# Performance work log

Hardware: AMD Instinct MI355X
Metric: run time of the kernel (lower is better)

## Reference

```python
import jax, jax.numpy as jnp
import numpy as np

POS_RATIO = 0.5
EPS = 1e-6


def setup_inputs() -> dict:
    key = jax.random.key(0)
    k1, k2, k3, k4 = jax.random.split(key, 4)
    N, C, D, H, W = 8, 256, 8, 16, 16
    q = jax.random.normal(k1, (N, C, D, H, W), dtype=jnp.float32)
    k = jax.random.normal(k2, (N, C, D, H, W), dtype=jnp.float32)
    # coords: (x0, y0, z0, x1, y1, z1) with lower-right > upper-left
    uq = jax.random.uniform(k3, (N, 3), dtype=jnp.float32) * 0.5
    uk = jax.random.uniform(k4, (N, 3), dtype=jnp.float32) * 0.5
    coord_q = jnp.concatenate([uq, uq + 0.5], axis=1)
    coord_k = jnp.concatenate([uk, uk + 0.5], axis=1)
    return {"q": q, "k": k, "coord_q": coord_q, "coord_k": coord_k}


def _centers(coord, D, H, W):
    """Per-batch voxel-center coordinates. coord: [N,6]. Returns cx, cy, cz each [N, D*H*W], plus bin diag [N]."""
    bw = (coord[:, 3] - coord[:, 0]) / W  # [N]
    bh = (coord[:, 4] - coord[:, 1]) / H
    bd = (coord[:, 5] - coord[:, 2]) / D
    gz, gy, gx = jnp.meshgrid(jnp.arange(D, dtype=coord.dtype),
                              jnp.arange(H, dtype=coord.dtype),
                              jnp.arange(W, dtype=coord.dtype), indexing="ij")
    gx = (gx + 0.5).reshape(-1)[None, :]  # [1, DHW]
    gy = (gy + 0.5).reshape(-1)[None, :]
    gz = (gz + 0.5).reshape(-1)[None, :]
    cx = gx * bw[:, None] + coord[:, 0][:, None]
    cy = gy * bh[:, None] + coord[:, 1][:, None]
    cz = gz * bd[:, None] + coord[:, 2][:, None]
    diag = jnp.sqrt(bw ** 2 + bh ** 2 + bd ** 2)  # [N]
    return cx, cy, cz, diag


def reference(q, k, coord_q, coord_k):
    N, C, D, H, W = q.shape
    qf = q.reshape(N, C, -1)  # [N, C, P], P = D*H*W
    kf = k.reshape(N, C, -1)
    cqx, cqy, cqz, q_diag = _centers(coord_q, D, H, W)
    ckx, cky, ckz, k_diag = _centers(coord_k, D, H, W)
    max_diag = jnp.maximum(q_diag, k_diag)  # [N]
    # pairwise center distance, normalized by max bin diagonal: [N, P, P]
    dist = jnp.sqrt((cqx[:, :, None] - ckx[:, None, :]) ** 2
                    + (cqy[:, :, None] - cky[:, None, :]) ** 2
                    + (cqz[:, :, None] - ckz[:, None, :]) ** 2) / max_diag[:, None, None]
    pos_mask = jax.lax.stop_gradient((dist < POS_RATIO).astype(q.dtype))
    # logit[n, p, p'] = sum_c q[n,c,p] * k[n,c,p']
    logit = jnp.einsum("ncp,ncq->npq", qf, kf)
    loss = (logit * pos_mask).sum((-2, -1)) / (pos_mask.sum((-2, -1)) + EPS)  # [N]
    return -2.0 * loss.mean()
```

## Files before the change

### kernel.cpp

```cpp
#include <hip/hip_runtime.h>
#include <cstdint>
#include <cstddef>

#define NB 8
#define CH 256
#define DD 8
#define HH 16
#define WW 16
#define PP 2048

#define OFF_DPART 8192

__device__ __forceinline__ int z_window(float czq, float bdk, float k2, float maxd) {
    float lim = 0.500060f * maxd;
    int zk0 = -1;
    #pragma unroll
    for (int zk = 0; zk < DD; ++zk) {
        float czk = __fadd_rn(__fmul_rn(__fadd_rn((float)zk, 0.5f), bdk), k2);
        bool feas = fabsf(__fsub_rn(czq, czk)) < lim;
        if (feas && zk0 < 0) zk0 = zk;
    }
    if (zk0 > DD - 2) zk0 = DD - 2;
    return zk0;
}

#define CC 8
__global__ __launch_bounds__(256) void fused_kernel(
    const float* __restrict__ q, const float* __restrict__ k,
    const float* __restrict__ coord_q, const float* __restrict__ coord_k,
    float* __restrict__ partial, float* __restrict__ dpart)
{
    __shared__ float klds[CC][512];
    __shared__ float redf[256];
    __shared__ int   redi[256];

    int t  = threadIdx.x;
    int cg = blockIdx.x;
    int zq = blockIdx.y;
    int n  = blockIdx.z;
    int flat = (n * 8 + zq) * 32 + cg;
    int c0 = cg * CC;

    const float* cq = coord_q + n * 6;
    const float* ck = coord_k + n * 6;
    float q0 = cq[0], q1 = cq[1], q2 = cq[2];
    float k0 = ck[0], k1 = ck[1], k2 = ck[2];
    float bwq = __fdiv_rn(__fsub_rn(cq[3], q0), (float)WW);
    float bhq = __fdiv_rn(__fsub_rn(cq[4], q1), (float)HH);
    float bdq = __fdiv_rn(__fsub_rn(cq[5], q2), (float)DD);
    float bwk = __fdiv_rn(__fsub_rn(ck[3], k0), (float)WW);
    float bhk = __fdiv_rn(__fsub_rn(ck[4], k1), (float)HH);
    float bdk = __fdiv_rn(__fsub_rn(ck[5], k2), (float)DD);
    float diagq = __fsqrt_rn(__fadd_rn(__fadd_rn(__fmul_rn(bwq, bwq), __fmul_rn(bhq, bhq)),
                                       __fmul_rn(bdq, bdq)));
    float diagk = __fsqrt_rn(__fadd_rn(__fadd_rn(__fmul_rn(bwk, bwk), __fmul_rn(bhk, bhk)),
                                       __fmul_rn(bdk, bdk)));
    float maxd = fmaxf(diagq, diagk);
    float cqz = __fadd_rn(__fmul_rn(__fadd_rn((float)zq, 0.5f), bdq), q2);

    int zk0 = z_window(cqz, bdk, k2, maxd);
    if (zk0 < 0) {
        if (t == 0) {
            partial[flat] = 0.0f;
            if (cg == 0) dpart[n * 8 + zq] = 0.0f;
        }
        return;
    }
    int base_p = zk0 << 8;

    {
        const float* ksrc = k + ((size_t)(n * CH + c0)) * PP + base_p;
        #pragma unroll
        for (int i = 0; i < 4; ++i) {
            int f = i * 256 + t;
            int c = f >> 7;
            int u = (f & 127) << 2;
            float4 v = *(const float4*)(ksrc + (size_t)c * PP + u);
            klds[c][u + 0] = v.x;
            klds[c][u + 1] = v.y;
            klds[c][u + 2] = v.z;
            klds[c][u + 3] = v.w;
        }
    }
    __syncthreads();

    int ix = t & 15, iy = (t >> 4) & 15;
    float cqx = __fadd_rn(__fmul_rn(__fadd_rn((float)ix, 0.5f), bwq), q0);
    float cqy = __fadd_rn(__fmul_rn(__fadd_rn((float)iy, 0.5f), bhq), q1);

    float lim = 0.500060f * maxd;
    float tx = (cqx - k0) / bwk - 0.5f;
    float ty = (cqy - k1) / bhk - 0.5f;
    float rx = lim / bwk + 0.03f;
    float ry = lim / bhk + 0.03f;
    int jx0 = (int)ceilf(tx - rx);  if (jx0 < 0) jx0 = 0;
    int jx1 = (int)floorf(tx + rx); if (jx1 > WW - 1) jx1 = WW - 1;
    int jy0 = (int)ceilf(ty - ry);  if (jy0 < 0) jy0 = 0;
    int jy1 = (int)floorf(ty + ry); if (jy1 > HH - 1) jy1 = HH - 1;

    float half_maxd = 0.5f * maxd;
    float thr2 = half_maxd * half_maxd * 1.001f;

    float s[CC];
    #pragma unroll
    for (int c = 0; c < CC; ++c) s[c] = 0.0f;
    int cnt = 0;

    for (int dzI = 0; dzI < 2; ++dzI) {
        int jz = zk0 + dzI;
        float ckz = __fadd_rn(__fmul_rn(__fadd_rn((float)jz, 0.5f), bdk), k2);
        float dz  = __fsub_rn(cqz, ckz);
        float dz2 = __fmul_rn(dz, dz);
        for (int jy = jy0; jy <= jy1; ++jy) {
            float cky = __fadd_rn(__fmul_rn(__fadd_rn((float)jy, 0.5f), bhk), k1);
            float dy  = __fsub_rn(cqy, cky);
            float dy2 = __fmul_rn(dy, dy);
            for (int jx = jx0; jx <= jx1; ++jx) {
                float ckx = __fadd_rn(__fmul_rn(__fadd_rn((float)jx, 0.5f), bwk), k0);
                float dx  = __fsub_rn(cqx, ckx);
                float dx2 = __fmul_rn(dx, dx);
                float d2  = __fadd_rn(__fadd_rn(dx2, dy2), dz2);
                bool pos = false;
                if (d2 < thr2) {
                    float dist = __fdiv_rn(__fsqrt_rn(d2), maxd);
                    pos = dist < 0.5f;
                }
                if (pos) {
                    ++cnt;
                    int idx = (dzI << 8) + (jy << 4) + jx;
                    #pragma unroll
                    for (int c = 0; c < CC; ++c)
                        s[c] += klds[c][idx];
                }
            }
        }
    }

    int p = (zq << 8) + t;
    float acc = 0.0f;
    const float* qcol = q + ((size_t)(n * CH + c0)) * PP + p;
    #pragma unroll
    for (int c = 0; c < CC; ++c)
        acc += qcol[(size_t)c * PP] * s[c];

    redf[t] = acc;
    redi[t] = cnt;
    __syncthreads();
    for (int off = 128; off > 0; off >>= 1) {
        if (t < off) { redf[t] += redf[t + off]; redi[t] += redi[t + off]; }
        __syncthreads();
    }
    if (t == 0) {
        partial[flat] = redf[0];
        if (cg == 0) dpart[n * 8 + zq] = (float)redi[0];
    }
}

__global__ __launch_bounds__(512) void final_kernel(const float* __restrict__ partial,
                                                    const float* __restrict__ dpart,
                                                    float* __restrict__ out)
{
    __shared__ float numsh[NB];
    __shared__ float densh[NB];
    int t = threadIdx.x;
    int n = t >> 6, lane = t & 63;

    float sp = 0.0f;
    #pragma unroll
    for (int i = 0; i < 4; ++i)
        sp += partial[n * 256 + i * 64 + lane];
    float sc = (lane < 8) ? dpart[n * 8 + lane] : 0.0f;
    for (int off = 32; off > 0; off >>= 1) {
        sp += __shfl_down(sp, off, 64);
        sc += __shfl_down(sc, off, 64);
    }
    if (lane == 0) { numsh[n] = sp; densh[n] = sc; }
    __syncthreads();
    if (t == 0) {
        float r = 0.0f;
        for (int i = 0; i < NB; ++i)
            r += numsh[i] / (densh[i] + 1e-6f);
        out[0] = -2.0f * (r / (float)NB);
    }
}

extern "C" void kernel_launch(void* const* d_in, const int* in_sizes, int n_in,
                              void* d_out, int out_size, void* d_ws, size_t ws_size,
                              hipStream_t stream) {
    const float* q       = (const float*)d_in[0];
    const float* k       = (const float*)d_in[1];
    const float* coord_q = (const float*)d_in[2];
    const float* coord_k = (const float*)d_in[3];
    float* out = (float*)d_out;

    char* w = (char*)d_ws;
    float* partial = (float*)w;
    float* dpart   = (float*)(w + OFF_DPART);

    fused_kernel<<<dim3(CH / CC, DD, NB), 256, 0, stream>>>(q, k, coord_q, coord_k,
                                                            partial, dpart);
    final_kernel<<<1, 512, 0, stream>>>(partial, dpart, out);
}
```

Before: 82.57 us.

## Double channels per block, prefetch q early, replace LDS reduction with wave shuffles

Doubles the channels handled per block from 8 to 16, which halves the grid and doubles per-block work. It also reuses each thread's neighbour-window distance computation across more channels. The q values are loaded into registers before the k tile is staged, so their global-load latency overlaps the LDS fill and the window search. The shared-memory tree reduction with its many barriers is replaced by per-wave shuffle reductions that write four partials per block, and the final kernel is adjusted to match. The cost is more registers and LDS per block, which can lower occupancy, and fewer blocks (1024) to spread across CUs.

```diff
diff --git a/kernel.cpp b/kernel.cpp
--- a/kernel.cpp
+++ b/kernel.cpp
@@ -9,7 +9,7 @@
 #define WW 16
 #define PP 2048
 
-#define OFF_DPART 8192
+#define OFF_DPART 16384
 
 __device__ __forceinline__ int z_window(float czq, float bdk, float k2, float maxd) {
     float lim = 0.500060f * maxd;
@@ -24,21 +24,21 @@
     return zk0;
 }
 
-#define CC 8
+#define CC 16
 __global__ __launch_bounds__(256) void fused_kernel(
     const float* __restrict__ q, const float* __restrict__ k,
     const float* __restrict__ coord_q, const float* __restrict__ coord_k,
     float* __restrict__ partial, float* __restrict__ dpart)
 {
     __shared__ float klds[CC][512];
-    __shared__ float redf[256];
-    __shared__ int   redi[256];
 
     int t  = threadIdx.x;
+    int wv = t >> 6;
+    int lane = t & 63;
     int cg = blockIdx.x;
     int zq = blockIdx.y;
     int n  = blockIdx.z;
-    int flat = (n * 8 + zq) * 32 + cg;
+    int flat = (n * 8 + zq) * 16 + cg;
     int c0 = cg * CC;
 
     const float* cq = coord_q + n * 6;
@@ -60,18 +60,27 @@
 
     int zk0 = z_window(cqz, bdk, k2, maxd);
     if (zk0 < 0) {
-        if (t == 0) {
-            partial[flat] = 0.0f;
-            if (cg == 0) dpart[n * 8 + zq] = 0.0f;
+        if (lane == 0) {
+            partial[flat * 4 + wv] = 0.0f;
+            if (cg == 0) dpart[(n * 8 + zq) * 4 + wv] = 0.0f;
         }
         return;
     }
     int base_p = zk0 << 8;
+
+    int p = (zq << 8) + t;
+    float qv[CC];
+    {
+        const float* qcol = q + ((size_t)(n * CH + c0)) * PP + p;
+        #pragma unroll
+        for (int c = 0; c < CC; ++c)
+            qv[c] = qcol[(size_t)c * PP];
+    }
 
     {
         const float* ksrc = k + ((size_t)(n * CH + c0)) * PP + base_p;
         #pragma unroll
-        for (int i = 0; i < 4; ++i) {
+        for (int i = 0; i < 8; ++i) {
             int f = i * 256 + t;
             int c = f >> 7;
             int u = (f & 127) << 2;
@@ -136,23 +145,20 @@
         }
     }
 
-    int p = (zq << 8) + t;
     float acc = 0.0f;
-    const float* qcol = q + ((size_t)(n * CH + c0)) * PP + p;
     #pragma unroll
     for (int c = 0; c < CC; ++c)
-        acc += qcol[(size_t)c * PP] * s[c];
-
-    redf[t] = acc;
-    redi[t] = cnt;
-    __syncthreads();
-    for (int off = 128; off > 0; off >>= 1) {
-        if (t < off) { redf[t] += redf[t + off]; redi[t] += redi[t + off]; }
-        __syncthreads();
-    }
-    if (t == 0) {
-        partial[flat] = redf[0];
-        if (cg == 0) dpart[n * 8 + zq] = (float)redi[0];
+        acc += qv[c] * s[c];
+
+    int ci = cnt;
+    #pragma unroll
+    for (int off = 32; off > 0; off >>= 1) {
+        acc += __shfl_down(acc, off, 64);
+        ci  += __shfl_down(ci, off, 64);
+    }
+    if (lane == 0) {
+        partial[flat * 4 + wv] = acc;
+        if (cg == 0) dpart[(n * 8 + zq) * 4 + wv] = (float)ci;
     }
 }
 
@@ -167,9 +173,10 @@
 
     float sp = 0.0f;
     #pragma unroll
-    for (int i = 0; i < 4; ++i)
-        sp += partial[n * 256 + i * 64 + lane];
-    float sc = (lane < 8) ? dpart[n * 8 + lane] : 0.0f;
+    for (int i = 0; i < 8; ++i)
+        sp += partial[n * 512 + i * 64 + lane];
+    float sc = (lane < 32) ? dpart[n * 32 + lane] : 0.0f;
+    #pragma unroll
     for (int off = 32; off > 0; off >>= 1) {
         sp += __shfl_down(sp, off, 64);
         sc += __shfl_down(sc, off, 64);
```

New measurement: 80.39 us. 1.03x faster.
